# Performance work log

Hardware: AMD Instinct MI355X
Metric: run time of the kernel (lower is better)

Reference implementation:

```python
import jax, jax.numpy as jnp
import numpy as np

BS, S, D, H = 2, 2048, 1024, 16
DH = D // H  # 64


def setup_inputs() -> dict:
    key = jax.random.key(0)
    k1, k2, k3 = jax.random.split(key, 3)
    x = jax.random.normal(k1, (BS, S, D), dtype=jnp.float32)
    w_qkv = jax.random.normal(k2, (D, H, 3 * DH), dtype=jnp.float32) * (D ** -0.5)
    b_qkv = jnp.zeros((H, 3 * DH), dtype=jnp.float32)
    w_out = jax.random.normal(k3, (H, DH, D), dtype=jnp.float32) * (D ** -0.5)
    b_out = jnp.zeros((D,), dtype=jnp.float32)
    return {"x": x, "w_qkv": w_qkv, "b_qkv": b_qkv, "w_out": w_out, "b_out": b_out}


def reference(x, w_qkv, b_qkv, w_out, b_out):
    dtype = x.dtype
    # QKV projection: DenseGeneral(features=(H, 3*DH)) -> [B, S, H, 3*DH]
    qkv = jnp.einsum("bsd,dhf->bshf", x, w_qkv) + b_qkv
    q, k, v = jnp.split(qkv, 3, axis=-1)  # each [B, S, H, DH]

    scale = DH ** -0.5
    q = (q * scale).astype(jnp.float32)
    k = k.astype(jnp.float32)
    # Full causal attention with fp32 scores (as in original)
    weights = jnp.einsum("bqhd,bkhd->bhqk", q, k)  # [B, H, S, S]
    causal = jnp.tril(jnp.ones((S, S), dtype=bool))[None, None, :, :]
    weights = jnp.where(causal, weights, jnp.finfo(jnp.float32).min)
    weights = jax.nn.softmax(weights, axis=-1).astype(dtype)
    attn = jnp.einsum("bhqk,bkhd->bqhd", weights, v).astype(dtype)

    # Output projection: DenseGeneral(D, axis=(-2, -1))
    out = jnp.einsum("bqhd,hdo->bqo", attn, w_out) + b_out
    return out
```

## Files before the change

### kernel.cpp

```cpp
#include <hip/hip_runtime.h>
#include <hip/hip_bf16.h>
#include <stdint.h>

#define NBS 2
#define SEQ 2048
#define DMODEL 1024
#define NH 16
#define DHEAD 64
#define MROWS (NBS*SEQ)
#define NQKV (NH*3*DHEAD)

typedef __bf16 bf16;
typedef __bf16 bf16x8 __attribute__((ext_vector_type(8)));
typedef float f32x4 __attribute__((ext_vector_type(4)));
typedef float f32x16 __attribute__((ext_vector_type(16)));
typedef unsigned int u32x2 __attribute__((ext_vector_type(2)));

#define LOG2E 1.44269504088896f
#define QSCALE (0.125f * LOG2E)

static __device__ __forceinline__ void gload_lds16(const bf16* g, bf16* l) {
    __builtin_amdgcn_global_load_lds(
        (const __attribute__((address_space(1))) uint32_t*)g,
        (__attribute__((address_space(3))) uint32_t*)l, 16, 0, 0);
}

static __device__ __forceinline__ bf16x8 ld_b8(const bf16* p) {
    return __builtin_bit_cast(bf16x8, *(const uint4*)p);
}

static __device__ __forceinline__ uint32_t pk_bf16(float lo, float hi) {
    unsigned short l = __builtin_bit_cast(unsigned short, (bf16)lo);
    unsigned short h = __builtin_bit_cast(unsigned short, (bf16)hi);
    return ((uint32_t)h << 16) | (uint32_t)l;
}

static __device__ __forceinline__ u32x2 lane_swap32(uint32_t a, uint32_t b, int lane) {
#if __has_builtin(__builtin_amdgcn_permlane32_swap)
    return __builtin_amdgcn_permlane32_swap(a, b, false, false);
#else
    uint32_t sa = __shfl_xor(a, 32), sb = __shfl_xor(b, 32);
    u32x2 r;
    r.x = (lane >= 32) ? sb : a;
    r.y = (lane >= 32) ? b : sa;
    return r;
#endif
}


__global__ void k_cvt(const float* __restrict__ in, bf16* __restrict__ out, int n4) {
    int i = blockIdx.x * blockDim.x + threadIdx.x;
    if (i < n4) {
        float4 v = ((const float4*)in)[i];
        ushort4 o;
        o.x = __builtin_bit_cast(unsigned short, (bf16)v.x);
        o.y = __builtin_bit_cast(unsigned short, (bf16)v.y);
        o.z = __builtin_bit_cast(unsigned short, (bf16)v.z);
        o.w = __builtin_bit_cast(unsigned short, (bf16)v.w);
        ((ushort4*)out)[i] = o;
    }
}

__global__ void k_tcvt(const float* __restrict__ in, bf16* __restrict__ out, int R, int C) {
    __shared__ float t[32][33];
    int tx = threadIdx.x, ty = threadIdx.y;
    int r0 = blockIdx.y * 32, c0 = blockIdx.x * 32;
#pragma unroll
    for (int i = 0; i < 4; i++)
        t[ty + i*8][tx] = in[(size_t)(r0 + ty + i*8) * C + (c0 + tx)];
    __syncthreads();
#pragma unroll
    for (int i = 0; i < 4; i++)
        out[(size_t)(c0 + ty + i*8) * R + (r0 + tx)] = (bf16)t[tx][ty + i*8];
}

template<int KD>
static __device__ __forceinline__ void gemm_tile(
        const bf16* __restrict__ A, const bf16* __restrict__ Bt,
        bf16* As, bf16* Bs, f32x4 acc[4][4], int tile_m, int tile_n) {
    int tid = threadIdx.x;
    int wave = tid >> 6, lane = tid & 63;
    int wr = wave >> 1, wc = wave & 1;
    int g = lane >> 4, r = lane & 15;
    int srow = lane >> 2, schunk = (lane & 3) * 8;

#pragma unroll
    for (int m = 0; m < 4; m++)
#pragma unroll
        for (int n = 0; n < 4; n++)
            acc[m][n] = (f32x4){0.f, 0.f, 0.f, 0.f};

    for (int k0 = 0; k0 < KD; k0 += 32) {
#pragma unroll
        for (int i = 0; i < 2; i++) {
            int ii = wave + i * 4;
            gload_lds16(A  + (size_t)(tile_m + ii*16 + srow) * KD + k0 + schunk, As + ii*512);
            gload_lds16(Bt + (size_t)(tile_n + ii*16 + srow) * KD + k0 + schunk, Bs + ii*512);
        }
        __syncthreads();
        bf16x8 af[4], bfr[4];
#pragma unroll
        for (int m = 0; m < 4; m++) af[m]  = *(const bf16x8*)(As + (wr*64 + m*16 + r)*32 + g*8);
#pragma unroll
        for (int n = 0; n < 4; n++) bfr[n] = *(const bf16x8*)(Bs + (wc*64 + n*16 + r)*32 + g*8);
#pragma unroll
        for (int m = 0; m < 4; m++)
#pragma unroll
            for (int n = 0; n < 4; n++)
                acc[m][n] = __builtin_amdgcn_mfma_f32_16x16x32_bf16(af[m], bfr[n], acc[m][n], 0, 0, 0);
        __syncthreads();
    }
}

__global__ __launch_bounds__(256) void k_gemm_qkv(
        const bf16* __restrict__ A, const bf16* __restrict__ Bt,
        const float* __restrict__ bias,
        bf16* __restrict__ Q, bf16* __restrict__ Kp, bf16* __restrict__ Vt) {
    __shared__ __align__(16) bf16 As[128*32];
    __shared__ __align__(16) bf16 Bs[128*32];
    f32x4 acc[4][4];
    int tile_m = blockIdx.y * 128, tile_n = blockIdx.x * 128;
    gemm_tile<DMODEL>(A, Bt, As, Bs, acc, tile_m, tile_n);

    int wave = threadIdx.x >> 6, lane = threadIdx.x & 63;
    int wr = wave >> 1, wc = wave & 1, g = lane >> 4, r = lane & 15;
#pragma unroll
    for (int m = 0; m < 4; m++) {
#pragma unroll
        for (int n = 0; n < 4; n++) {
            int col = tile_n + wc*64 + n*16 + r;
            int h = col / 192, f = col % 192;
            int kind = f >> 6, d = f & 63;
            float bv = bias[col];
#pragma unroll
            for (int j = 0; j < 4; j++) {
                int row = tile_m + wr*64 + m*16 + g*4 + j;
                int b = row >> 11, s = row & 2047;
                float v = acc[m][n][j] + bv;
                if (kind == 0) {
                    Q[(((size_t)(b*NH + h)) * SEQ + s) * DHEAD + d] = (bf16)(v * QSCALE);
                } else if (kind == 1) {
                    Kp[(((size_t)(b*NH + h)) * SEQ + s) * DHEAD + d] = (bf16)v;
                } else {
                    Vt[(((size_t)(b*NH + h)) * DHEAD + d) * SEQ + s] = (bf16)v;
                }
            }
        }
    }
}

__global__ __launch_bounds__(256) void k_gemm_out(
        const bf16* __restrict__ A, const bf16* __restrict__ Bt,
        const float* __restrict__ bias, float* __restrict__ out) {
    __shared__ __align__(16) bf16 As[128*32];
    __shared__ __align__(16) bf16 Bs[128*32];
    f32x4 acc[4][4];
    int tile_m = blockIdx.y * 128, tile_n = blockIdx.x * 128;
    gemm_tile<DMODEL>(A, Bt, As, Bs, acc, tile_m, tile_n);

    int wave = threadIdx.x >> 6, lane = threadIdx.x & 63;
    int wr = wave >> 1, wc = wave & 1, g = lane >> 4, r = lane & 15;
#pragma unroll
    for (int m = 0; m < 4; m++) {
#pragma unroll
        for (int n = 0; n < 4; n++) {
            int col = tile_n + wc*64 + n*16 + r;
            float bv = bias[col];
#pragma unroll
            for (int j = 0; j < 4; j++) {
                int row = tile_m + wr*64 + m*16 + g*4 + j;
                out[(size_t)row * DMODEL + col] = acc[m][n][j] + bv;
            }
        }
    }
}

#define QBLK 128
#define KVB 64

__global__ __launch_bounds__(256) void k_attn(
        const bf16* __restrict__ Q, const bf16* __restrict__ K,
        const bf16* __restrict__ Vt, bf16* __restrict__ O) {
    int bh = blockIdx.y;
    int qc = (bh >= 16) ? (15 - (int)blockIdx.x) : (int)blockIdx.x;
    int q0 = qc * QBLK;
    int tid = threadIdx.x, wave = tid >> 6, lane = tid & 63;
    int l31 = lane & 31, hi = lane >> 5;

    __shared__ __align__(16) bf16 Ks[2][KVB*72];
    __shared__ __align__(16) bf16 VsT[2][KVB*72];

    const bf16* Kg = K  + (size_t)bh * SEQ * DHEAD;
    const bf16* Vg = Vt + (size_t)bh * DHEAD * SEQ;

    int qb = q0 + wave * 32;
    int qrow = qb + l31;

    const bf16* qrow_p = Q + ((size_t)bh * SEQ + qrow) * DHEAD;
    bf16x8 qa2[4];
#pragma unroll
    for (int c = 0; c < 4; c++) qa2[c] = ld_b8(qrow_p + c*16 + hi*8);

    const f32x16 z16 = {0,0,0,0,0,0,0,0,0,0,0,0,0,0,0,0};
    f32x16 o32[2];
    o32[0] = z16; o32[1] = z16;
    float l_part = 0.f;

    int nt = 2*qc + 2;
    int qmax_wave = qb + 31;

    int krow0 = tid >> 3, kseg0 = (tid & 7) * 8;
    int krow1 = krow0 + 32;
    int vd0 = tid >> 3, vseg0 = (tid & 7) * 8;
    int vd1 = vd0 + 32;

    bf16x8 kreg[2], vreg[2];
    kreg[0] = ld_b8(Kg + (size_t)krow0 * DHEAD + kseg0);
    kreg[1] = ld_b8(Kg + (size_t)krow1 * DHEAD + kseg0);
    vreg[0] = ld_b8(Vg + (size_t)vd0 * SEQ + vseg0);
    vreg[1] = ld_b8(Vg + (size_t)vd1 * SEQ + vseg0);

    int cur = 0;
    for (int t = 0; t < nt; t++) {
        int kv0 = t * KVB;
        *(uint4*)&Ks[cur][krow0*72 + kseg0]  = __builtin_bit_cast(uint4, kreg[0]);
        *(uint4*)&Ks[cur][krow1*72 + kseg0]  = __builtin_bit_cast(uint4, kreg[1]);
        *(uint4*)&VsT[cur][vd0*72 + vseg0]   = __builtin_bit_cast(uint4, vreg[0]);
        *(uint4*)&VsT[cur][vd1*72 + vseg0]   = __builtin_bit_cast(uint4, vreg[1]);
        __syncthreads();

        if (t + 1 < nt) {
            int kv1 = kv0 + KVB;
            kreg[0] = ld_b8(Kg + (size_t)(kv1 + krow0) * DHEAD + kseg0);
            kreg[1] = ld_b8(Kg + (size_t)(kv1 + krow1) * DHEAD + kseg0);
            vreg[0] = ld_b8(Vg + (size_t)vd0 * SEQ + kv1 + vseg0);
            vreg[1] = ld_b8(Vg + (size_t)vd1 * SEQ + kv1 + vseg0);
        }

        if (kv0 <= qmax_wave) {
            f32x16 st[2];
            st[0] = z16; st[1] = z16;
            __builtin_amdgcn_s_setprio(1);
#pragma unroll
            for (int c = 0; c < 4; c++) {
#pragma unroll
                for (int rb = 0; rb < 2; rb++) {
                    bf16x8 kf = ld_b8(&Ks[cur][(rb*32 + l31)*72 + c*16 + hi*8]);
                    st[rb] = __builtin_amdgcn_mfma_f32_32x32x16_bf16(kf, qa2[c], st[rb], 0, 0, 0);
                }
            }
            __builtin_amdgcn_s_setprio(0);

            bf16x8 vf[2][4];
#pragma unroll
            for (int dblk = 0; dblk < 2; dblk++)
#pragma unroll
                for (int c = 0; c < 4; c++)
                    vf[dblk][c] = ld_b8(&VsT[cur][(dblk*32 + l31)*72 + c*16 + hi*8]);

            bool needm = (kv0 + KVB - 1) > qb;
            float l_add = 0.f;
#pragma unroll
            for (int rb = 0; rb < 2; rb++) {
#pragma unroll
                for (int reg = 0; reg < 16; reg++) {
                    float e = __builtin_amdgcn_exp2f(st[rb][reg]);
                    if (needm) {
                        int kv = kv0 + rb*32 + (reg & 3) + 8*(reg >> 2) + 4*hi;
                        if (kv > qrow) e = 0.f;
                    }
                    l_add += e;
                    st[rb][reg] = e;
                }
            }
            l_part += l_add;

            bf16x8 pa[4];
#pragma unroll
            for (int c = 0; c < 4; c++) {
                const f32x16& pp = st[c >> 1];
                const int base = (c & 1) * 8;
                uint32_t a0 = pk_bf16(pp[base+0], pp[base+1]);
                uint32_t a1 = pk_bf16(pp[base+2], pp[base+3]);
                uint32_t b0 = pk_bf16(pp[base+4], pp[base+5]);
                uint32_t b1 = pk_bf16(pp[base+6], pp[base+7]);
                u32x2 s0 = lane_swap32(a0, b0, lane);
                u32x2 s1 = lane_swap32(a1, b1, lane);
                uint4 fr = {s0.x, s1.x, s0.y, s1.y};
                pa[c] = __builtin_bit_cast(bf16x8, fr);
            }

            __builtin_amdgcn_s_setprio(1);
#pragma unroll
            for (int dblk = 0; dblk < 2; dblk++)
#pragma unroll
                for (int c = 0; c < 4; c++)
                    o32[dblk] = __builtin_amdgcn_mfma_f32_32x32x16_bf16(pa[c], vf[dblk][c], o32[dblk], 0, 0, 0);
            __builtin_amdgcn_s_setprio(0);
        }
        cur ^= 1;
    }

    l_part += __shfl_xor(l_part, 32);
    float linv = 1.0f / l_part;

    float lrv[16];
#pragma unroll
    for (int reg = 0; reg < 16; reg++) {
        int qr = (reg & 3) + 8*(reg >> 2) + 4*hi;
        lrv[reg] = __shfl(linv, qr);
    }

    int b = bh >> 4, h = bh & 15;
#pragma unroll
    for (int reg = 0; reg < 16; reg++) {
        int qr = (reg & 3) + 8*(reg >> 2) + 4*hi;
        int srow = q0 + wave*32 + qr;
        size_t base = (((size_t)b * SEQ + srow) * NH + h) * DHEAD + l31;
        O[base]      = (bf16)(o32[0][reg] * lrv[reg]);
        O[base + 32] = (bf16)(o32[1][reg] * lrv[reg]);
    }
}


extern "C" void kernel_launch(void* const* d_in, const int* in_sizes, int n_in,
                              void* d_out, int out_size, void* d_ws, size_t ws_size,
                              hipStream_t stream) {
    const float* x     = (const float*)d_in[0];
    const float* w_qkv = (const float*)d_in[1];
    const float* b_qkv = (const float*)d_in[2];
    const float* w_out = (const float*)d_in[3];
    const float* b_out = (const float*)d_in[4];
    float* out = (float*)d_out;

    char* ws = (char*)d_ws;
    bf16* xb   = (bf16*)(ws);
    bf16* wqkT = (bf16*)(ws + 8388608);
    bf16* woT  = (bf16*)(ws + 14680064);
    bf16* qb   = (bf16*)(ws + 16777216);
    bf16* kb   = (bf16*)(ws + 25165824);
    bf16* vb   = (bf16*)(ws + 33554432);
    bf16* attn = xb;

    k_cvt<<<(MROWS*DMODEL/4 + 255)/256, 256, 0, stream>>>(x, xb, MROWS*DMODEL/4);
    dim3 tb(32, 8);
    k_tcvt<<<dim3(NQKV/32, DMODEL/32), tb, 0, stream>>>(w_qkv, wqkT, DMODEL, NQKV);
    k_tcvt<<<dim3(DMODEL/32, DMODEL/32), tb, 0, stream>>>(w_out, woT, DMODEL, DMODEL);

    k_gemm_qkv<<<dim3(NQKV/128, MROWS/128), 256, 0, stream>>>(xb, wqkT, b_qkv, qb, kb, vb);
    k_attn<<<dim3(SEQ/QBLK, NBS*NH), 256, 0, stream>>>(qb, kb, vb, attn);
    k_gemm_out<<<dim3(DMODEL/128, MROWS/128), 256, 0, stream>>>(attn, woT, b_out, out);
}
```

Measured before the change: 129.1 us.

## Split attention KV range in two with merge kernel; permute QKV weight columns

Each causal query block's KV range is split into two halves handled by separate workgroups, which write unnormalised partial outputs and row sums that a new merge kernel combines and normalises. This balances the uneven causal work and doubles the number of workgroups. The QKV weight transpose also permutes columns so that Q, K and V are contiguous column groups, which simplifies the GEMM epilogue index math. In exchange it adds extra global traffic for the partials, an extra kernel launch, and bf16 rounding of partial outputs before the merge.

New measurement: 146.9 us. 13.7% more time.

```diff
diff --git a/kernel.cpp b/kernel.cpp
--- a/kernel.cpp
+++ b/kernel.cpp
@@ -74,6 +74,23 @@
         out[(size_t)(c0 + ty + i*8) * R + (r0 + tx)] = (bf16)t[tx][ty + i*8];
 }
 
+__global__ void k_tcvt_qkv(const float* __restrict__ in, bf16* __restrict__ out) {
+    __shared__ float t[32][33];
+    int tx = threadIdx.x, ty = threadIdx.y;
+    int r0 = blockIdx.y * 32, c0 = blockIdx.x * 32;
+#pragma unroll
+    for (int i = 0; i < 4; i++)
+        t[ty + i*8][tx] = in[(size_t)(r0 + ty + i*8) * NQKV + (c0 + tx)];
+    __syncthreads();
+#pragma unroll
+    for (int i = 0; i < 4; i++) {
+        int c = c0 + ty + i*8;
+        int h = c / 192, f = c % 192;
+        int cperm = ((f >> 6) << 10) + (h << 6) + (f & 63);
+        out[(size_t)cperm * DMODEL + (r0 + tx)] = (bf16)t[tx][ty + i*8];
+    }
+}
+
 template<int KD>
 static __device__ __forceinline__ void gemm_tile(
         const bf16* __restrict__ A, const bf16* __restrict__ Bt,
@@ -129,9 +146,10 @@
 #pragma unroll
         for (int n = 0; n < 4; n++) {
             int col = tile_n + wc*64 + n*16 + r;
-            int h = col / 192, f = col % 192;
-            int kind = f >> 6, d = f & 63;
-            float bv = bias[col];
+            int kind = col >> 10;
+            int h = (col >> 6) & 15;
+            int d = col & 63;
+            float bv = bias[h*192 + (kind << 6) + d];
 #pragma unroll
             for (int j = 0; j < 4; j++) {
                 int row = tile_m + wr*64 + m*16 + g*4 + j;
@@ -178,6 +196,178 @@
 #define QBLK 128
 #define KVB 64
 
+static __device__ __forceinline__ void attn_tile_body(
+        const bf16* Ks, const bf16* VsT,
+        const bf16x8 qa2[4], f32x16 o32[2], float& l_part,
+        int kv0, int qb, int qrow, int l31, int hi, int lane) {
+    const f32x16 z16 = {0,0,0,0,0,0,0,0,0,0,0,0,0,0,0,0};
+    f32x16 st[2];
+    st[0] = z16; st[1] = z16;
+    __builtin_amdgcn_s_setprio(1);
+#pragma unroll
+    for (int c = 0; c < 4; c++) {
+#pragma unroll
+        for (int rb = 0; rb < 2; rb++) {
+            bf16x8 kf = ld_b8(&Ks[(rb*32 + l31)*72 + c*16 + hi*8]);
+            st[rb] = __builtin_amdgcn_mfma_f32_32x32x16_bf16(kf, qa2[c], st[rb], 0, 0, 0);
+        }
+    }
+    __builtin_amdgcn_s_setprio(0);
+
+    bf16x8 vf[2][4];
+#pragma unroll
+    for (int dblk = 0; dblk < 2; dblk++)
+#pragma unroll
+        for (int c = 0; c < 4; c++)
+            vf[dblk][c] = ld_b8(&VsT[(dblk*32 + l31)*72 + c*16 + hi*8]);
+
+    bool needm = (kv0 + KVB - 1) > qb;
+    float l4[4] = {0.f, 0.f, 0.f, 0.f};
+#pragma unroll
+    for (int rb = 0; rb < 2; rb++) {
+#pragma unroll
+        for (int reg = 0; reg < 16; reg++) {
+            float e = __builtin_amdgcn_exp2f(st[rb][reg]);
+            if (needm) {
+                int kv = kv0 + rb*32 + (reg & 3) + 8*(reg >> 2) + 4*hi;
+                if (kv > qrow) e = 0.f;
+            }
+            l4[reg & 3] += e;
+            st[rb][reg] = e;
+        }
+    }
+    l_part += (l4[0] + l4[1]) + (l4[2] + l4[3]);
+
+    bf16x8 pa[4];
+#pragma unroll
+    for (int c = 0; c < 4; c++) {
+        const f32x16& pp = st[c >> 1];
+        const int base = (c & 1) * 8;
+        uint32_t a0 = pk_bf16(pp[base+0], pp[base+1]);
+        uint32_t a1 = pk_bf16(pp[base+2], pp[base+3]);
+        uint32_t b0 = pk_bf16(pp[base+4], pp[base+5]);
+        uint32_t b1 = pk_bf16(pp[base+6], pp[base+7]);
+        u32x2 s0 = lane_swap32(a0, b0, lane);
+        u32x2 s1 = lane_swap32(a1, b1, lane);
+        uint4 fr = {s0.x, s1.x, s0.y, s1.y};
+        pa[c] = __builtin_bit_cast(bf16x8, fr);
+    }
+
+    __builtin_amdgcn_s_setprio(1);
+#pragma unroll
+    for (int dblk = 0; dblk < 2; dblk++)
+#pragma unroll
+        for (int c = 0; c < 4; c++)
+            o32[dblk] = __builtin_amdgcn_mfma_f32_32x32x16_bf16(pa[c], vf[dblk][c], o32[dblk], 0, 0, 0);
+    __builtin_amdgcn_s_setprio(0);
+}
+
+__global__ __launch_bounds__(256) void k_attn_split(
+        const bf16* __restrict__ Q, const bf16* __restrict__ K,
+        const bf16* __restrict__ Vt,
+        bf16* __restrict__ Op, float* __restrict__ Lp) {
+    int bh = blockIdx.y;
+    int x = blockIdx.x;
+    int qc = x >> 1, half = x & 1;
+    int q0 = qc * QBLK;
+    int tid = threadIdx.x, wave = tid >> 6, lane = tid & 63;
+    int l31 = lane & 31, hi = lane >> 5;
+
+    __shared__ __align__(16) bf16 Ks[2][KVB*72];
+    __shared__ __align__(16) bf16 VsT[2][KVB*72];
+
+    const bf16* Kg = K  + (size_t)bh * SEQ * DHEAD;
+    const bf16* Vg = Vt + (size_t)bh * DHEAD * SEQ;
+
+    int qb = q0 + wave * 32;
+    int qrow = qb + l31;
+
+    const bf16* qrow_p = Q + ((size_t)bh * SEQ + qrow) * DHEAD;
+    bf16x8 qa2[4];
+#pragma unroll
+    for (int c = 0; c < 4; c++) qa2[c] = ld_b8(qrow_p + c*16 + hi*8);
+
+    const f32x16 z16 = {0,0,0,0,0,0,0,0,0,0,0,0,0,0,0,0};
+    f32x16 o32[2];
+    o32[0] = z16; o32[1] = z16;
+    float l_part = 0.f;
+
+    int t0 = half * (qc + 1);
+    int t1 = t0 + (qc + 1);
+    int qmax_wave = qb + 31;
+
+    int krow0 = tid >> 3, kseg0 = (tid & 7) * 8;
+    int krow1 = krow0 + 32;
+    int vd0 = tid >> 3, vseg0 = (tid & 7) * 8;
+    int vd1 = vd0 + 32;
+
+    bf16x8 kreg[2], vreg[2];
+    {
+        int kvs = t0 * KVB;
+        kreg[0] = ld_b8(Kg + (size_t)(kvs + krow0) * DHEAD + kseg0);
+        kreg[1] = ld_b8(Kg + (size_t)(kvs + krow1) * DHEAD + kseg0);
+        vreg[0] = ld_b8(Vg + (size_t)vd0 * SEQ + kvs + vseg0);
+        vreg[1] = ld_b8(Vg + (size_t)vd1 * SEQ + kvs + vseg0);
+    }
+
+    int cur = 0;
+    for (int t = t0; t < t1; t++) {
+        int kv0 = t * KVB;
+        *(uint4*)&Ks[cur][krow0*72 + kseg0]  = __builtin_bit_cast(uint4, kreg[0]);
+        *(uint4*)&Ks[cur][krow1*72 + kseg0]  = __builtin_bit_cast(uint4, kreg[1]);
+        *(uint4*)&VsT[cur][vd0*72 + vseg0]   = __builtin_bit_cast(uint4, vreg[0]);
+        *(uint4*)&VsT[cur][vd1*72 + vseg0]   = __builtin_bit_cast(uint4, vreg[1]);
+        __syncthreads();
+
+        if (t + 1 < t1) {
+            int kv1 = kv0 + KVB;
+            kreg[0] = ld_b8(Kg + (size_t)(kv1 + krow0) * DHEAD + kseg0);
+            kreg[1] = ld_b8(Kg + (size_t)(kv1 + krow1) * DHEAD + kseg0);
+            vreg[0] = ld_b8(Vg + (size_t)vd0 * SEQ + kv1 + vseg0);
+            vreg[1] = ld_b8(Vg + (size_t)vd1 * SEQ + kv1 + vseg0);
+        }
+
+        if (kv0 <= qmax_wave)
+            attn_tile_body(Ks[cur], VsT[cur], qa2, o32, l_part,
+                           kv0, qb, qrow, l31, hi, lane);
+        cur ^= 1;
+    }
+
+    l_part += __shfl_xor(l_part, 32);
+    if (hi == 0)
+        Lp[half*65536 + bh*SEQ + qrow] = l_part;
+
+    size_t ob = (size_t)half * 4194304;
+#pragma unroll
+    for (int reg = 0; reg < 16; reg++) {
+        int qr = (reg & 3) + 8*(reg >> 2) + 4*hi;
+        int srow = q0 + wave*32 + qr;
+        size_t base = ob + ((size_t)bh * SEQ + srow) * DHEAD + l31;
+        Op[base]      = (bf16)o32[0][reg];
+        Op[base + 32] = (bf16)o32[1][reg];
+    }
+}
+
+__global__ __launch_bounds__(256) void k_merge(
+        const bf16* __restrict__ Op, const float* __restrict__ Lp,
+        bf16* __restrict__ Oa) {
+    int g = blockIdx.x * 256 + threadIdx.x;
+    int dseg = g & 7;
+    int s = (g >> 3) & 2047;
+    int bh = g >> 14;
+    size_t ro = ((size_t)bh * SEQ + s) * DHEAD + dseg*8;
+    bf16x8 p0 = ld_b8(Op + ro);
+    bf16x8 p1 = ld_b8(Op + 4194304 + ro);
+    float inv = 1.0f / (Lp[bh*SEQ + s] + Lp[65536 + bh*SEQ + s]);
+    bf16x8 r;
+#pragma unroll
+    for (int j = 0; j < 8; j++)
+        r[j] = (bf16)(((float)p0[j] + (float)p1[j]) * inv);
+    int b = bh >> 4, h = bh & 15;
+    *(uint4*)&Oa[(((size_t)b * SEQ + s) * NH + h) * DHEAD + dseg*8] =
+        __builtin_bit_cast(uint4, r);
+}
+
 __global__ __launch_bounds__(256) void k_attn(
         const bf16* __restrict__ Q, const bf16* __restrict__ K,
         const bf16* __restrict__ Vt, bf16* __restrict__ O) {
@@ -237,67 +427,9 @@
             vreg[1] = ld_b8(Vg + (size_t)vd1 * SEQ + kv1 + vseg0);
         }
 
-        if (kv0 <= qmax_wave) {
-            f32x16 st[2];
-            st[0] = z16; st[1] = z16;
-            __builtin_amdgcn_s_setprio(1);
-#pragma unroll
-            for (int c = 0; c < 4; c++) {
-#pragma unroll
-                for (int rb = 0; rb < 2; rb++) {
-                    bf16x8 kf = ld_b8(&Ks[cur][(rb*32 + l31)*72 + c*16 + hi*8]);
-                    st[rb] = __builtin_amdgcn_mfma_f32_32x32x16_bf16(kf, qa2[c], st[rb], 0, 0, 0);
-                }
-            }
-            __builtin_amdgcn_s_setprio(0);
-
-            bf16x8 vf[2][4];
-#pragma unroll
-            for (int dblk = 0; dblk < 2; dblk++)
-#pragma unroll
-                for (int c = 0; c < 4; c++)
-                    vf[dblk][c] = ld_b8(&VsT[cur][(dblk*32 + l31)*72 + c*16 + hi*8]);
-
-            bool needm = (kv0 + KVB - 1) > qb;
-            float l_add = 0.f;
-#pragma unroll
-            for (int rb = 0; rb < 2; rb++) {
-#pragma unroll
-                for (int reg = 0; reg < 16; reg++) {
-                    float e = __builtin_amdgcn_exp2f(st[rb][reg]);
-                    if (needm) {
-                        int kv = kv0 + rb*32 + (reg & 3) + 8*(reg >> 2) + 4*hi;
-                        if (kv > qrow) e = 0.f;
-                    }
-                    l_add += e;
-                    st[rb][reg] = e;
-                }
-            }
-            l_part += l_add;
-
-            bf16x8 pa[4];
-#pragma unroll
-            for (int c = 0; c < 4; c++) {
-                const f32x16& pp = st[c >> 1];
-                const int base = (c & 1) * 8;
-                uint32_t a0 = pk_bf16(pp[base+0], pp[base+1]);
-                uint32_t a1 = pk_bf16(pp[base+2], pp[base+3]);
-                uint32_t b0 = pk_bf16(pp[base+4], pp[base+5]);
-                uint32_t b1 = pk_bf16(pp[base+6], pp[base+7]);
-                u32x2 s0 = lane_swap32(a0, b0, lane);
-                u32x2 s1 = lane_swap32(a1, b1, lane);
-                uint4 fr = {s0.x, s1.x, s0.y, s1.y};
-                pa[c] = __builtin_bit_cast(bf16x8, fr);
-            }
-
-            __builtin_amdgcn_s_setprio(1);
-#pragma unroll
-            for (int dblk = 0; dblk < 2; dblk++)
-#pragma unroll
-                for (int c = 0; c < 4; c++)
-                    o32[dblk] = __builtin_amdgcn_mfma_f32_32x32x16_bf16(pa[c], vf[dblk][c], o32[dblk], 0, 0, 0);
-            __builtin_amdgcn_s_setprio(0);
-        }
+        if (kv0 <= qmax_wave)
+            attn_tile_body(Ks[cur], VsT[cur], qa2, o32, l_part,
+                           kv0, qb, qrow, l31, hi, lane);
         cur ^= 1;
     }
 
@@ -340,14 +472,24 @@
     bf16* qb   = (bf16*)(ws + 16777216);
     bf16* kb   = (bf16*)(ws + 25165824);
     bf16* vb   = (bf16*)(ws + 33554432);
+    bf16* Opart = (bf16*)(ws + 41943040);
+    float* Lpart = (float*)(ws + 58720256);
+    const size_t WS_NEED = 59244544;
     bf16* attn = xb;
 
     k_cvt<<<(MROWS*DMODEL/4 + 255)/256, 256, 0, stream>>>(x, xb, MROWS*DMODEL/4);
     dim3 tb(32, 8);
-    k_tcvt<<<dim3(NQKV/32, DMODEL/32), tb, 0, stream>>>(w_qkv, wqkT, DMODEL, NQKV);
+    k_tcvt_qkv<<<dim3(NQKV/32, DMODEL/32), tb, 0, stream>>>(w_qkv, wqkT);
     k_tcvt<<<dim3(DMODEL/32, DMODEL/32), tb, 0, stream>>>(w_out, woT, DMODEL, DMODEL);
 
     k_gemm_qkv<<<dim3(NQKV/128, MROWS/128), 256, 0, stream>>>(xb, wqkT, b_qkv, qb, kb, vb);
-    k_attn<<<dim3(SEQ/QBLK, NBS*NH), 256, 0, stream>>>(qb, kb, vb, attn);
+
+    if (ws_size >= WS_NEED) {
+        k_attn_split<<<dim3(32, NBS*NH), 256, 0, stream>>>(qb, kb, vb, Opart, Lpart);
+        k_merge<<<(NBS*NH*SEQ*DHEAD/8)/256, 256, 0, stream>>>(Opart, Lpart, attn);
+    } else {
+        k_attn<<<dim3(SEQ/QBLK, NBS*NH), 256, 0, stream>>>(qb, kb, vb, attn);
+    }
+
     k_gemm_out<<<dim3(DMODEL/128, MROWS/128), 256, 0, stream>>>(attn, woT, b_out, out);
 }
```
